# Kernel optimization log

Measured on AMD Instinct MI355X. Metric: run time of the kernel, lower is better.

## Reference

```python
import jax, jax.numpy as jnp
import numpy as np

D_MODEL = 1024
N_HEADS = 16
HEAD_DIM = D_MODEL // N_HEADS
B, T = 4, 2048
EPS = 1e-5


def _layernorm(x, w, b):
    mu = jnp.mean(x, axis=-1, keepdims=True)
    var = jnp.mean(jnp.square(x - mu), axis=-1, keepdims=True)
    return (x - mu) * jax.lax.rsqrt(var + EPS) * w + b


def _heads(x, w, b):
    # x: [B,T,D]; w stored [in,out] so y = x @ w + b (== torch Linear)
    y = x @ w + b
    return y.reshape(B, T, N_HEADS, HEAD_DIM).transpose(0, 2, 1, 3)  # [B,H,T,hd]


def _attention(q, k, v):
    scores = jnp.einsum('bhqd,bhkd->bhqk', q, k) / np.sqrt(HEAD_DIM).astype(np.float32)
    attn = jax.nn.softmax(scores, axis=-1)  # dropout is identity in eval mode
    o = jnp.einsum('bhqk,bhkd->bhqd', attn, v)
    return o.transpose(0, 2, 1, 3).reshape(B, T, D_MODEL)


def setup_inputs() -> dict:
    key = jax.random.key(0)
    ks = jax.random.split(key, 16)
    s = 1.0 / np.sqrt(D_MODEL)
    def lin(k, din, dout):
        kw, kb = jax.random.split(k)
        return (jax.random.uniform(kw, (din, dout), jnp.float32, -s, s),
                jax.random.uniform(kb, (dout,), jnp.float32, -s, s))
    inp = {}
    inp['temporal_tokens'] = jax.random.normal(ks[0], (B, T, D_MODEL), jnp.float32)
    inp['feature_tokens'] = jax.random.normal(ks[1], (B, T, D_MODEL), jnp.float32)
    names = ['qt', 'kf', 'vf', 'qf', 'kt', 'vt', 'ot', 'of']
    for i, n in enumerate(names):
        w, b = lin(ks[2 + i], D_MODEL, D_MODEL)
        inp[n + '_w'], inp[n + '_b'] = w, b
    inp['fus1_w'], inp['fus1_b'] = lin(ks[10], 2 * D_MODEL, D_MODEL)
    inp['fus2_w'], inp['fus2_b'] = lin(ks[11], D_MODEL, D_MODEL)
    for n in ['ln_fus', 'ln_t', 'ln_f']:
        inp[n + '_w'] = jnp.ones((D_MODEL,), jnp.float32)
        inp[n + '_b'] = jnp.zeros((D_MODEL,), jnp.float32)
    return inp


def reference(temporal_tokens, feature_tokens,
              qt_w, qt_b, kf_w, kf_b, vf_w, vf_b,
              qf_w, qf_b, kt_w, kt_b, vt_w, vt_b,
              ot_w, ot_b, of_w, of_b,
              fus1_w, fus1_b, fus2_w, fus2_b,
              ln_fus_w, ln_fus_b, ln_t_w, ln_t_b, ln_f_w, ln_f_b):
    # temporal -> feature cross attention
    Qt = _heads(temporal_tokens, qt_w, qt_b)
    Kf = _heads(feature_tokens, kf_w, kf_b)
    Vf = _heads(feature_tokens, vf_w, vf_b)
    attn_t = _attention(Qt, Kf, Vf) @ ot_w + ot_b
    fused_t = _layernorm(temporal_tokens + attn_t, ln_t_w, ln_t_b)
    # feature -> temporal cross attention
    Qf = _heads(feature_tokens, qf_w, qf_b)
    Kt = _heads(temporal_tokens, kt_w, kt_b)
    Vt = _heads(temporal_tokens, vt_w, vt_b)
    attn_f = _attention(Qf, Kt, Vt) @ of_w + of_b
    fused_f = _layernorm(feature_tokens + attn_f, ln_f_w, ln_f_b)
    # fusion MLP
    combined = jnp.concatenate([fused_t, fused_f], axis=-1)  # [B,T,2D]
    h = jax.nn.gelu(combined @ fus1_w + fus1_b, approximate=False)
    fused = _layernorm(h @ fus2_w + fus2_b, ln_fus_w, ln_fus_b)
    return fused
```

## Files before the change

### kernel.cpp

```cpp
#include <hip/hip_runtime.h>
#include <math.h>

typedef __attribute__((ext_vector_type(8))) short short8;
typedef __attribute__((ext_vector_type(4))) short short4v;
typedef __attribute__((ext_vector_type(4))) float floatx4;
typedef __attribute__((ext_vector_type(16))) float floatx16;

#define GLOBAL_AS __attribute__((address_space(1)))
#define LDS_AS __attribute__((address_space(3)))

__device__ __forceinline__ float bf2f(unsigned short u) {
    unsigned int x = ((unsigned int)u) << 16;
    return __builtin_bit_cast(float, x);
}
__device__ __forceinline__ unsigned short f2bf(float f) {
    unsigned int u = __builtin_bit_cast(unsigned int, f);
    u += 0x7fffu + ((u >> 16) & 1u);
    return (unsigned short)(u >> 16);
}

struct WX {
    const float* src[10];
    unsigned long long dst[10];
    int r64[10];
    int cum[11];
};

__global__ __launch_bounds__(256) void prep_kernel(
    WX P, unsigned short* __restrict__ base,
    const float* __restrict__ ta, const float* __restrict__ tb,
    unsigned short* __restrict__ oa, unsigned short* __restrict__ ob)
{
    __shared__ unsigned short T[64][72];
    const int bx = blockIdx.x;
    if (bx >= P.cum[10]) {
        const int cb = bx - P.cum[10];
        const float* in = cb < 1024 ? ta : tb;
        unsigned short* out = cb < 1024 ? oa : ob;
        const size_t b0 = (size_t)(cb & 1023) * 8192;
        #pragma unroll
        for (int j = 0; j < 8; ++j) {
            const size_t i = b0 + (size_t)j * 1024 + threadIdx.x * 4;
            float4 f = *(const float4*)(in + i);
            unsigned short o[4] = {f2bf(f.x), f2bf(f.y), f2bf(f.z), f2bf(f.w)};
            *(uint2*)(out + i) = *(const uint2*)o;
        }
        return;
    }
    int w = 0;
    #pragma unroll
    for (int i = 0; i < 10; ++i) if (bx >= P.cum[i + 1]) w = i + 1;
    const int tix = bx - P.cum[w];
    const int R = P.r64[w] * 64;
    const int r0 = (tix >> 4) * 64, c0 = (tix & 15) * 64;
    const float* in = P.src[w];
    unsigned short* out = base + P.dst[w];
    const int t = threadIdx.x;
    {
        const int r = t >> 2, cc = (t & 3) * 16;
        const float* p = in + (size_t)(r0 + r) * 1024 + c0 + cc;
        #pragma unroll
        for (int j = 0; j < 16; j += 4) {
            float4 f = *(const float4*)(p + j);
            T[cc + j + 0][r] = f2bf(f.x);
            T[cc + j + 1][r] = f2bf(f.y);
            T[cc + j + 2][r] = f2bf(f.z);
            T[cc + j + 3][r] = f2bf(f.w);
        }
    }
    __syncthreads();
    {
        const int c = t >> 2, rr = (t & 3) * 16;
        unsigned short* q = out + (size_t)(c0 + c) * R + r0 + rr;
        *(uint4*)(q)     = *(const uint4*)(&T[c][rr]);
        *(uint4*)(q + 8) = *(const uint4*)(&T[c][rr + 8]);
    }
}

#define G256_DECL(A_, B_, Kdim)                                               \
    const int tid = threadIdx.x;                                              \
    const int wave = tid >> 6, lane = tid & 63;                               \
    const int quad = lane >> 4, l16 = lane & 15;                              \
    const int wr = wave >> 2, wc = wave & 3;                                  \
    const int lrow8 = lane >> 3, lc8 = lane & 7;                              \
    floatx4 acc[8][4];                                                        \
    _Pragma("unroll")                                                         \
    for (int i = 0; i < 8; ++i)                                               \
        _Pragma("unroll")                                                     \
        for (int j = 0; j < 4; ++j) acc[i][j] = (floatx4){0.f, 0.f, 0.f, 0.f}; \
    const unsigned short* sA[4];                                              \
    const unsigned short* sB[4];                                              \
    int ldst[4];                                                              \
    _Pragma("unroll")                                                         \
    for (int h = 0; h < 2; ++h)                                               \
        _Pragma("unroll")                                                     \
        for (int j = 0; j < 2; ++j) {                                         \
            const int r0 = h * 128 + j * 64 + wave * 8;                       \
            const int r = r0 + lrow8;                                         \
            const int cg = lc8 ^ (r & 7);                                     \
            sA[h * 2 + j] = (A_) + (size_t)(bm + r) * (Kdim) + cg * 8;        \
            sB[h * 2 + j] = (B_) + (size_t)(bn + r) * (Kdim) + cg * 8;        \
            ldst[h * 2 + j] = r0 * 64;                                        \
        }

#define G256_STG_A(s_) __builtin_amdgcn_global_load_lds(                      \
    (const GLOBAL_AS void*)(sA[s_] + ko), (LDS_AS void*)(L + cb + ldst[s_]), 16, 0, 0)
#define G256_STG_B(s_) __builtin_amdgcn_global_load_lds(                      \
    (const GLOBAL_AS void*)(sB[s_] + ko), (LDS_AS void*)(L + cb + 16384 + ldst[s_]), 16, 0, 0)

#define G256_LDA(mh_)                                                         \
    _Pragma("unroll")                                                         \
    for (int mi = 0; mi < 4; ++mi) {                                          \
        const int r = (mh_) * 128 + wr * 64 + mi * 16 + l16;                  \
        _Pragma("unroll")                                                     \
        for (int kk = 0; kk < 2; ++kk)                                        \
            afc[mi][kk] = *(const short8*)&L[cb + r * 64 +                    \
                (((kk * 4 + quad) ^ (r & 7)) * 8)];                           \
    }
#define G256_LDB(nh_)                                                         \
    _Pragma("unroll")                                                         \
    for (int nj = 0; nj < 2; ++nj) {                                          \
        const int r = (nh_) * 128 + wc * 32 + nj * 16 + l16;                  \
        _Pragma("unroll")                                                     \
        for (int kk = 0; kk < 2; ++kk)                                        \
            bfr[(nh_) * 2 + nj][kk] = *(const short8*)&L[cb + 16384 + r * 64 +\
                (((kk * 4 + quad) ^ (r & 7)) * 8)];                           \
    }

#define G256_FENCE() do {                                                     \
    asm volatile("s_waitcnt lgkmcnt(0)" ::: "memory");                        \
    __builtin_amdgcn_sched_barrier(0);                                        \
    __builtin_amdgcn_s_barrier(); } while (0)

#define G256_MM(mh_, nb_) do {                                                \
    __builtin_amdgcn_s_setprio(1);                                            \
    _Pragma("unroll")                                                         \
    for (int mi = 0; mi < 4; ++mi)                                            \
        _Pragma("unroll")                                                     \
        for (int nj = 0; nj < 2; ++nj)                                        \
            _Pragma("unroll")                                                 \
            for (int kk = 0; kk < 2; ++kk)                                    \
                acc[(mh_) * 4 + mi][(nb_) + nj] =                             \
                    __builtin_amdgcn_mfma_f32_16x16x32_bf16(                  \
                        bfr[(nb_) + nj][kk], afc[mi][kk],                     \
                        acc[(mh_) * 4 + mi][(nb_) + nj], 0, 0, 0);            \
    __builtin_amdgcn_s_setprio(0); } while (0)

#define G256_CORE(A_, B_, Kdim)                                               \
    G256_DECL(A_, B_, Kdim)                                                   \
    {                       \
        _Pragma("unroll")                                                     \
        for (int s = 0; s < 4; ++s) {                                         \
            __builtin_amdgcn_global_load_lds((const GLOBAL_AS void*)(sA[s]),  \
                (LDS_AS void*)(L + ldst[s]), 16, 0, 0);                       \
            __builtin_amdgcn_global_load_lds((const GLOBAL_AS void*)(sB[s]),  \
                (LDS_AS void*)(L + 16384 + ldst[s]), 16, 0, 0);               \
        }                                                                     \
        _Pragma("unroll")                                                     \
        for (int s = 0; s < 4; ++s) {                                         \
            __builtin_amdgcn_global_load_lds((const GLOBAL_AS void*)(sA[s] + 64), \
                (LDS_AS void*)(L + 32768 + ldst[s]), 16, 0, 0);               \
            __builtin_amdgcn_global_load_lds((const GLOBAL_AS void*)(sB[s] + 64), \
                (LDS_AS void*)(L + 32768 + 16384 + ldst[s]), 16, 0, 0);       \
        }                                                                     \
        asm volatile("s_waitcnt vmcnt(8)" ::: "memory");                      \
        __builtin_amdgcn_s_barrier();                                         \
    }                                                                         \
    short8 afc[4][2];                                                         \
    short8 bfr[4][2];                                                         \
    const int NT = (Kdim) >> 6;                                               \
    for (int t = 0; t < NT; ++t) {                                            \
        const int cb = (t & 1) << 15;                                         \
        const int ko = (t + 2) << 6;                                          \
        const bool stg = (t < NT - 2);                                        \
                                                                      \
        G256_LDA(0)                                                           \
        G256_LDB(0)                                                           \
        G256_FENCE();                                                         \
        G256_MM(0, 0);                                                        \
                                                                      \
        G256_LDB(1)                                                           \
        if (stg) { G256_STG_A(0); G256_STG_A(1); G256_STG_B(0); G256_STG_B(1); } \
        G256_FENCE();                                                         \
        G256_MM(0, 2);                                                        \
                                                                      \
        G256_LDA(1)                                                           \
        if (stg) { G256_STG_B(2); G256_STG_B(3); }                            \
        G256_FENCE();                                                         \
        G256_MM(1, 2);                                                        \
                                                                      \
        if (stg) {                                                            \
            G256_STG_A(2); G256_STG_A(3);                                     \
            asm volatile("s_waitcnt vmcnt(8)" ::: "memory");                  \
        } else {                                                              \
            asm volatile("s_waitcnt vmcnt(0)" ::: "memory");                  \
        }                                                                     \
        __builtin_amdgcn_sched_barrier(0);                                    \
        __builtin_amdgcn_s_barrier();                                         \
        G256_MM(1, 0);                                                        \
    }


template <int MODE>
__global__ __launch_bounds__(512, 2) void gemm_kernel(
    const unsigned short* __restrict__ A,
    const unsigned short* __restrict__ Wt,
    const float* __restrict__ bias,
    unsigned short* __restrict__ C,
    int N, int K)
{
    __shared__ unsigned short L[65536];
    const int bm = blockIdx.x * 256, bn = blockIdx.y * 256;
    G256_CORE(A, Wt, K)

    #pragma unroll
    for (int i = 0; i < 8; ++i) {
        const int m = bm + (i >> 2) * 128 + wr * 64 + (i & 3) * 16 + l16;
        #pragma unroll
        for (int j = 0; j < 4; ++j) {
            const int n0 = bn + (j >> 1) * 128 + wc * 32 + (j & 1) * 16 + quad * 4;
            float4 bv = *(const float4*)&bias[n0];
            float v[4];
            #pragma unroll
            for (int r = 0; r < 4; ++r)
                v[r] = acc[i][j][r] + ((const float*)&bv)[r];
            if (MODE == 2) {
                #pragma unroll
                for (int r = 0; r < 4; ++r)
                    v[r] = 0.5f * v[r] * (1.0f + erff(v[r] * 0.70710678118f));
            }
            unsigned short o[4] = {f2bf(v[0]), f2bf(v[1]), f2bf(v[2]), f2bf(v[3])};
            *(uint2*)&C[(size_t)m * N + n0] = *(const uint2*)o;
        }
    }
}

__global__ __launch_bounds__(512, 2) void gemm_out_kernel(
    const unsigned short* __restrict__ A0, const unsigned short* __restrict__ W0,
    const float* __restrict__ bi0, const float* __restrict__ r0, unsigned short* __restrict__ C0,
    const unsigned short* __restrict__ A1, const unsigned short* __restrict__ W1,
    const float* __restrict__ bi1, const float* __restrict__ r1, unsigned short* __restrict__ C1)
{
    __shared__ unsigned short L[65536];
    const int s1 = blockIdx.y >> 2;
    const unsigned short* A = s1 ? A1 : A0;
    const unsigned short* Wt = s1 ? W1 : W0;
    const float* bias = s1 ? bi1 : bi0;
    const float* resid = s1 ? r1 : r0;
    unsigned short* C = s1 ? C1 : C0;
    const int bm = blockIdx.x * 256, bn = (blockIdx.y & 3) * 256;
    G256_CORE(A, Wt, 1024)

    #pragma unroll
    for (int i = 0; i < 8; ++i) {
        const int m = bm + (i >> 2) * 128 + wr * 64 + (i & 3) * 16 + l16;
        #pragma unroll
        for (int j = 0; j < 4; ++j) {
            const int n0 = bn + (j >> 1) * 128 + wc * 32 + (j & 1) * 16 + quad * 4;
            float4 bv = *(const float4*)&bias[n0];
            float4 rv = *(const float4*)&resid[(size_t)m * 1024 + n0];
            float v[4];
            v[0] = acc[i][j][0] + bv.x + rv.x;
            v[1] = acc[i][j][1] + bv.y + rv.y;
            v[2] = acc[i][j][2] + bv.z + rv.z;
            v[3] = acc[i][j][3] + bv.w + rv.w;
            unsigned short o[4] = {f2bf(v[0]), f2bf(v[1]), f2bf(v[2]), f2bf(v[3])};
            *(uint2*)&C[(size_t)m * 1024 + n0] = *(const uint2*)o;
        }
    }
}

__global__ __launch_bounds__(512, 2) void gemm_qkv_kernel(
    const unsigned short* __restrict__ At, const unsigned short* __restrict__ Wt3t,
    const float* __restrict__ tb0, const float* __restrict__ tb1, const float* __restrict__ tb2,
    unsigned short* __restrict__ to0, unsigned short* __restrict__ to1, unsigned short* __restrict__ to2,
    const unsigned short* __restrict__ Af, const unsigned short* __restrict__ Wt3f,
    const float* __restrict__ fb0, const float* __restrict__ fb1, const float* __restrict__ fb2,
    unsigned short* __restrict__ fo0, unsigned short* __restrict__ fo1, unsigned short* __restrict__ fo2,
    float scale0)
{
    __shared__ unsigned short L[65536];
    const int str = blockIdx.y >= 12;
    const unsigned short* A = str ? Af : At;
    const unsigned short* Wt = str ? Wt3f : Wt3t;
    const int byy = str ? (blockIdx.y - 12) : blockIdx.y;
    const int buf = byy >> 2;
    const int bn = byy * 256;
    const int cn = (byy & 3) * 256;
    const float* bias = str ? (buf == 0 ? fb0 : (buf == 1 ? fb1 : fb2))
                            : (buf == 0 ? tb0 : (buf == 1 ? tb1 : tb2));
    unsigned short* C = str ? (buf == 0 ? fo0 : (buf == 1 ? fo1 : fo2))
                            : (buf == 0 ? to0 : (buf == 1 ? to1 : to2));
    const float scale = buf == 0 ? scale0 : 1.0f;
    const int bm = blockIdx.x * 256;
    G256_CORE(A, Wt, 1024)

    #pragma unroll
    for (int i = 0; i < 8; ++i) {
        const int m = bm + (i >> 2) * 128 + wr * 64 + (i & 3) * 16 + l16;
        #pragma unroll
        for (int j = 0; j < 4; ++j) {
            const int n0 = cn + (j >> 1) * 128 + wc * 32 + (j & 1) * 16 + quad * 4;
            float4 bv = *(const float4*)&bias[n0];
            unsigned short o[4];
            #pragma unroll
            for (int r = 0; r < 4; ++r)
                o[r] = f2bf((acc[i][j][r] + ((const float*)&bv)[r]) * scale);
            if (buf == 2) {
                const int b = m >> 11, tk = m & 2047;
                const int h = n0 >> 6, d0 = n0 & 63;
                const int tsw = tk ^ ((d0 & 8) ? 4 : 0);
                unsigned short* vb = C + ((size_t)(b * 16 + h) * 64) * 2048 + tsw;
                #pragma unroll
                for (int r = 0; r < 4; ++r) vb[(size_t)(d0 + r) * 2048] = o[r];
            } else {
                *(uint2*)&C[(size_t)m * 1024 + n0] = *(const uint2*)o;
            }
        }
    }
}

__global__ __launch_bounds__(256) void flash_kernel(
    const unsigned short* __restrict__ Q0, const unsigned short* __restrict__ K0,
    const unsigned short* __restrict__ V0, unsigned short* __restrict__ O0,
    const unsigned short* __restrict__ Q1, const unsigned short* __restrict__ K1,
    const unsigned short* __restrict__ V1, unsigned short* __restrict__ O1)
{
    __shared__ unsigned short Ks[64 * 64];
    __shared__ unsigned short Vs[64 * 64];

    const int bid = blockIdx.x;
    const int p = (bid & 7) * 16 + (bid >> 7);
    const int qt = (bid >> 3) & 15;
    const int s1 = p >= 64;
    const int rem = p & 63;
    const int b = rem >> 4, h = rem & 15;
    const unsigned short* Q = s1 ? Q1 : Q0;
    const unsigned short* Kmat = s1 ? K1 : K0;
    const unsigned short* Vtp = s1 ? V1 : V0;
    unsigned short* O = s1 ? O1 : O0;
    const int q0 = qt * 128;

    const int tid = threadIdx.x;
    const int wave = tid >> 6, lane = tid & 63;
    const int quad = lane >> 4, l16 = lane & 15;

    const unsigned short* qp = Q + (size_t)(b * 2048 + q0 + wave * 32 + l16) * 1024 + h * 64;
    short8 qf[2][2];
    qf[0][0] = *(const short8*)(qp + quad * 8);
    qf[0][1] = *(const short8*)(qp + 32 + quad * 8);
    qf[1][0] = *(const short8*)(qp + 16 * 1024 + quad * 8);
    qf[1][1] = *(const short8*)(qp + 16 * 1024 + 32 + quad * 8);

    const int srow8 = lane >> 3;
    const int c8 = lane & 7;
    const int rit0 = wave * 16 + srow8;
    const int rit1 = rit0 + 8;
    const int col0 = (c8 ^ (rit0 & 7)) * 8;
    const int col1 = (c8 ^ (rit1 & 7)) * 8;
    const unsigned short* kbase = Kmat + (size_t)b * 2048 * 1024 + h * 64;
    const unsigned short* vbase = Vtp + (size_t)(b * 16 + h) * 64 * 2048;
    unsigned short* lk0 = Ks + (wave * 16) * 64;
    unsigned short* lk1 = lk0 + 8 * 64;
    unsigned short* lv0 = Vs + (wave * 16) * 64;
    unsigned short* lv1 = lv0 + 8 * 64;

    int koff[4][2];
    #pragma unroll
    for (int nt = 0; nt < 4; ++nt)
        #pragma unroll
        for (int hh = 0; hh < 2; ++hh)
            koff[nt][hh] = (nt * 16 + l16) * 64 + (((hh * 4 + quad) ^ (l16 & 7)) * 8);
    int voff[4][4];
    #pragma unroll
    for (int dt = 0; dt < 4; ++dt)
        #pragma unroll
        for (int nt = 0; nt < 4; ++nt)
            voff[dt][nt] = (dt * 16 + l16) * 64 +
                           (((nt * 2 + (quad >> 1)) ^ (l16 & 7)) * 8) +
                           (((quad & 1) ^ (l16 >> 3)) * 4);

    floatx4 oa[2][4], la[2];
    #pragma unroll
    for (int qg = 0; qg < 2; ++qg) {
        la[qg] = (floatx4){0.f, 0.f, 0.f, 0.f};
        #pragma unroll
        for (int dt = 0; dt < 4; ++dt) oa[qg][dt] = (floatx4){0.f, 0.f, 0.f, 0.f};
    }
    const short4v vone = {(short)0x3F80, (short)0x3F80, (short)0x3F80, (short)0x3F80};

    for (int kt = 0; kt < 32; ++kt) {
        const unsigned short* kg0 = kbase + (size_t)(kt * 64 + rit0) * 1024 + col0;
        const unsigned short* kg1 = kbase + (size_t)(kt * 64 + rit1) * 1024 + col1;
        const unsigned short* vg0 = vbase + (size_t)rit0 * 2048 + kt * 64 + col0;
        const unsigned short* vg1 = vbase + (size_t)rit1 * 2048 + kt * 64 + col1;
        __builtin_amdgcn_global_load_lds((const GLOBAL_AS void*)kg0, (LDS_AS void*)lk0, 16, 0, 0);
        __builtin_amdgcn_global_load_lds((const GLOBAL_AS void*)kg1, (LDS_AS void*)lk1, 16, 0, 0);
        __builtin_amdgcn_global_load_lds((const GLOBAL_AS void*)vg0, (LDS_AS void*)lv0, 16, 0, 0);
        __builtin_amdgcn_global_load_lds((const GLOBAL_AS void*)vg1, (LDS_AS void*)lv1, 16, 0, 0);
        __syncthreads();

        short4v pf[2][4];
        #pragma unroll
        for (int nt = 0; nt < 4; ++nt) {
            short8 k0 = *(const short8*)&Ks[koff[nt][0]];
            short8 k1 = *(const short8*)&Ks[koff[nt][1]];
            #pragma unroll
            for (int qg = 0; qg < 2; ++qg) {
                floatx4 s = (floatx4){0.f, 0.f, 0.f, 0.f};
                s = __builtin_amdgcn_mfma_f32_16x16x32_bf16(k0, qf[qg][0], s, 0, 0, 0);
                s = __builtin_amdgcn_mfma_f32_16x16x32_bf16(k1, qf[qg][1], s, 0, 0, 0);
                float p0 = __builtin_amdgcn_exp2f(s[0]);
                float p1 = __builtin_amdgcn_exp2f(s[1]);
                float p2 = __builtin_amdgcn_exp2f(s[2]);
                float p3 = __builtin_amdgcn_exp2f(s[3]);
                union { unsigned u[2]; short4v s4; } pk;
                asm("v_cvt_pk_bf16_f32 %0, %1, %2"
                    : "=v"(pk.u[0]) : "v"(p0), "v"(p1));
                asm("v_cvt_pk_bf16_f32 %0, %1, %2"
                    : "=v"(pk.u[1]) : "v"(p2), "v"(p3));
                pf[qg][nt] = pk.s4;
                la[qg] = __builtin_amdgcn_mfma_f32_16x16x16bf16_1k(vone, pf[qg][nt], la[qg], 0, 0, 0);
            }
        }
        #pragma unroll
        for (int dt = 0; dt < 4; ++dt)
            #pragma unroll
            for (int nt = 0; nt < 4; ++nt) {
                short4v vf = *(const short4v*)&Vs[voff[dt][nt]];
                oa[0][dt] = __builtin_amdgcn_mfma_f32_16x16x16bf16_1k(vf, pf[0][nt], oa[0][dt], 0, 0, 0);
                oa[1][dt] = __builtin_amdgcn_mfma_f32_16x16x16bf16_1k(vf, pf[1][nt], oa[1][dt], 0, 0, 0);
            }
        __syncthreads();
    }

    #pragma unroll
    for (int qg = 0; qg < 2; ++qg) {
        const float linv = 1.0f / la[qg][0];
        unsigned short* orow = O + (size_t)(b * 2048 + q0 + wave * 32 + qg * 16 + l16) * 1024 + h * 64;
        #pragma unroll
        for (int dt = 0; dt < 4; ++dt) {
            unsigned short ob[4];
            #pragma unroll
            for (int r = 0; r < 4; ++r) ob[r] = f2bf(oa[qg][dt][r] * linv);
            *(uint2*)(orow + dt * 16 + quad * 4) = *(const uint2*)ob;
        }
    }
}

__global__ __launch_bounds__(256) void ln2_kernel(
    const unsigned short* __restrict__ in0, const unsigned short* __restrict__ in1,
    unsigned short* __restrict__ out,
    const float* __restrict__ w0, const float* __restrict__ b0,
    const float* __restrict__ w1, const float* __restrict__ b1)
{
    __shared__ float red[8];
    const int sel = blockIdx.x >> 13;
    const int row = blockIdx.x & 8191;
    const unsigned short* in = sel ? in1 : in0;
    const float* w = sel ? w1 : w0;
    const float* bb = sel ? b1 : b0;
    const int tid = threadIdx.x;
    const int wave = tid >> 6, lane = tid & 63;
    uint2 raw = *(const uint2*)(in + (size_t)row * 1024 + tid * 4);
    float v[4];
    v[0] = bf2f((unsigned short)(raw.x & 0xffffu));
    v[1] = bf2f((unsigned short)(raw.x >> 16));
    v[2] = bf2f((unsigned short)(raw.y & 0xffffu));
    v[3] = bf2f((unsigned short)(raw.y >> 16));
    float s = v[0] + v[1] + v[2] + v[3];
    float sq = v[0] * v[0] + v[1] * v[1] + v[2] * v[2] + v[3] * v[3];
    #pragma unroll
    for (int m = 1; m < 64; m <<= 1) { s += __shfl_xor(s, m); sq += __shfl_xor(sq, m); }
    if (lane == 0) { red[wave] = s; red[4 + wave] = sq; }
    __syncthreads();
    s = red[0] + red[1] + red[2] + red[3];
    sq = red[4] + red[5] + red[6] + red[7];
    const float mu = s * (1.0f / 1024.0f);
    const float var = sq * (1.0f / 1024.0f) - mu * mu;
    const float rstd = rsqrtf(var + 1e-5f);
    unsigned short ob[4];
    #pragma unroll
    for (int j = 0; j < 4; ++j)
        ob[j] = f2bf((v[j] - mu) * rstd * w[tid * 4 + j] + bb[tid * 4 + j]);
    *(uint2*)(out + (size_t)row * 2048 + sel * 1024 + tid * 4) = *(uint2*)ob;
}

__global__ __launch_bounds__(256) void ln_final_kernel(
    const unsigned short* __restrict__ in, float* __restrict__ out,
    const float* __restrict__ w, const float* __restrict__ bias)
{
    __shared__ float red[8];
    const int row = blockIdx.x;
    const int tid = threadIdx.x;
    const int wave = tid >> 6, lane = tid & 63;
    uint2 raw = *(const uint2*)(in + (size_t)row * 1024 + tid * 4);
    float v[4];
    v[0] = bf2f((unsigned short)(raw.x & 0xffffu));
    v[1] = bf2f((unsigned short)(raw.x >> 16));
    v[2] = bf2f((unsigned short)(raw.y & 0xffffu));
    v[3] = bf2f((unsigned short)(raw.y >> 16));
    float s = v[0] + v[1] + v[2] + v[3];
    float sq = v[0] * v[0] + v[1] * v[1] + v[2] * v[2] + v[3] * v[3];
    #pragma unroll
    for (int m = 1; m < 64; m <<= 1) { s += __shfl_xor(s, m); sq += __shfl_xor(sq, m); }
    if (lane == 0) { red[wave] = s; red[4 + wave] = sq; }
    __syncthreads();
    s = red[0] + red[1] + red[2] + red[3];
    sq = red[4] + red[5] + red[6] + red[7];
    const float mu = s * (1.0f / 1024.0f);
    const float var = sq * (1.0f / 1024.0f) - mu * mu;
    const float rstd = rsqrtf(var + 1e-5f);
    float o[4];
    #pragma unroll
    for (int j = 0; j < 4; ++j)
        o[j] = (v[j] - mu) * rstd * w[tid * 4 + j] + bias[tid * 4 + j];
    *(float4*)(out + (size_t)row * 1024 + tid * 4) = (float4){o[0], o[1], o[2], o[3]};
}

extern "C" void kernel_launch(void* const* d_in, const int* in_sizes, int n_in,
                              void* d_out, int out_size, void* d_ws, size_t ws_size,
                              hipStream_t stream)
{
    (void)in_sizes; (void)n_in; (void)out_size; (void)ws_size;
    const float* temporal = (const float*)d_in[0];
    const float* feature  = (const float*)d_in[1];
    const float* qt_w = (const float*)d_in[2];
    const float* qt_b = (const float*)d_in[3];
    const float* kf_w = (const float*)d_in[4];
    const float* kf_b = (const float*)d_in[5];
    const float* vf_w = (const float*)d_in[6];
    const float* vf_b = (const float*)d_in[7];
    const float* qf_w = (const float*)d_in[8];
    const float* qf_b = (const float*)d_in[9];
    const float* kt_w = (const float*)d_in[10];
    const float* kt_b = (const float*)d_in[11];
    const float* vt_w = (const float*)d_in[12];
    const float* vt_b = (const float*)d_in[13];
    const float* ot_w = (const float*)d_in[14];
    const float* ot_b = (const float*)d_in[15];
    const float* of_w = (const float*)d_in[16];
    const float* of_b = (const float*)d_in[17];
    const float* fus1_w = (const float*)d_in[18];
    const float* fus1_b = (const float*)d_in[19];
    const float* fus2_w = (const float*)d_in[20];
    const float* fus2_b = (const float*)d_in[21];
    const float* ln_fus_w = (const float*)d_in[22];
    const float* ln_fus_b = (const float*)d_in[23];
    const float* ln_t_w = (const float*)d_in[24];
    const float* ln_t_b = (const float*)d_in[25];
    const float* ln_f_w = (const float*)d_in[26];
    const float* ln_f_b = (const float*)d_in[27];

    unsigned short* p = (unsigned short*)d_ws;
    const size_t EW = 1024ull * 1024;
    const size_t ET = 8192ull * 1024;
    unsigned short* WT3t = p;
    unsigned short* WT3f = p + 3 * EW;
    unsigned short* WTot = p + 6 * EW;
    unsigned short* WTof = p + 7 * EW;
    unsigned short* WTf1 = p + 8 * EW;
    unsigned short* WTf2 = p + 10 * EW;
    size_t off = 11 * EW;
    unsigned short* Tb = p + off; off += ET;
    unsigned short* Fb = p + off; off += ET;
    unsigned short* Qt = p + off; off += ET;
    unsigned short* Kt = p + off; off += ET;
    unsigned short* Vt = p + off; off += ET;
    unsigned short* Qf = p + off; off += ET;
    unsigned short* Kf = p + off; off += ET;
    unsigned short* Vf = p + off; off += ET;
    unsigned short* VfT = p + off; off += ET;
    unsigned short* VtT = p + off; off += ET;
    unsigned short* attnT = p + off; off += ET;
    unsigned short* attnF = p + off; off += ET;
    unsigned short* yT = Qt;
    unsigned short* yF = Qf;
    unsigned short* comb = Kt;
    unsigned short* hbuf = Kf;
    unsigned short* y2 = Vf;
    (void)Vt;

    const float SC = 0.125f * 1.4426950408889634f;

    {
        WX P;
        const float* srcs[10] = {qt_w, kt_w, vt_w, qf_w, kf_w, vf_w,
                                 ot_w, of_w, fus1_w, fus2_w};
        unsigned long long dsts[10] = {
            0, EW, 2 * EW,
            3 * EW, 4 * EW, 5 * EW,
            6 * EW, 7 * EW, 8 * EW, 10 * EW};
        int cum = 0;
        P.cum[0] = 0;
        for (int i = 0; i < 10; ++i) {
            P.src[i] = srcs[i];
            P.dst[i] = dsts[i];
            P.r64[i] = (i == 8) ? 32 : 16;
            cum += P.r64[i] * 16;
            P.cum[i + 1] = cum;
        }
        prep_kernel<<<cum + 2048, 256, 0, stream>>>(P, p, temporal, feature, Tb, Fb);
    }

    const dim3 gb5(512);
    gemm_qkv_kernel<<<dim3(32, 24), gb5, 0, stream>>>(
        Tb, WT3t, qt_b, kt_b, vt_b, Qt, Kt, VtT,
        Fb, WT3f, qf_b, kf_b, vf_b, Qf, Kf, VfT, SC);
    flash_kernel<<<2048, dim3(256), 0, stream>>>(
        Qt, Kf, VfT, attnT, Qf, Kt, VtT, attnF);
    gemm_out_kernel<<<dim3(32, 8), gb5, 0, stream>>>(
        attnT, WTot, ot_b, temporal, yT,
        attnF, WTof, of_b, feature,  yF);
    ln2_kernel<<<16384, dim3(256), 0, stream>>>(yT, yF, comb, ln_t_w, ln_t_b, ln_f_w, ln_f_b);
    gemm_kernel<2><<<dim3(32, 4), gb5, 0, stream>>>(comb, WTf1, fus1_b, hbuf, 1024, 2048);
    gemm_kernel<0><<<dim3(32, 4), gb5, 0, stream>>>(hbuf, WTf2, fus2_b, y2, 1024, 1024);
    ln_final_kernel<<<8192, dim3(256), 0, stream>>>(y2, (float*)d_out, ln_fus_w, ln_fus_b);
}
```

Before: 660.3 us.

## Replace fusion MLP GEMMs with 128x128 tile kernel using 32x32 MFMA

The two fusion-MLP GEMMs move off the 256x256-tile, 512-thread pipelined core onto a new 128x128-tile, 256-thread kernel. It uses 32x32x16 bf16 MFMA, swizzled LDS and direct global-to-LDS loads. The grid grows from 128 to 512 blocks to fill the CUs better on these mid-sized GEMMs, but the new loop is single-buffered with no prefetch overlap. The flash kernel also replaces its precomputed per-tile K/V LDS offset arrays with base offsets plus a constant stride, which reduces register pressure.

Result: faster. 640.8 us, median of 3 (-3.0%).

```diff
diff --git a/kernel.cpp b/kernel.cpp
--- a/kernel.cpp
+++ b/kernel.cpp
@@ -74,6 +74,101 @@
         unsigned short* q = out + (size_t)(c0 + c) * R + r0 + rr;
         *(uint4*)(q)     = *(const uint4*)(&T[c][rr]);
         *(uint4*)(q + 8) = *(const uint4*)(&T[c][rr + 8]);
+    }
+}
+
+#define GEMM_CORE(A_, B_, Kdim)                                               \
+    const int tid = threadIdx.x;                                              \
+    const int wave = tid >> 6, lane = tid & 63;                               \
+    const int l32 = lane & 31, hi = lane >> 5;                                \
+    const int wm = (wave & 1) * 64, wn = (wave >> 1) * 64;                    \
+    const int srow8 = lane >> 3, c8 = lane & 7;                               \
+    const int scol = (c8 ^ srow8) * 8;                                        \
+    floatx16 acc[2][2];                                                       \
+    _Pragma("unroll")                                                         \
+    for (int i = 0; i < 2; ++i)                                               \
+        _Pragma("unroll")                                                     \
+        for (int j = 0; j < 2; ++j)                                           \
+            _Pragma("unroll")                                                 \
+            for (int r = 0; r < 16; ++r) acc[i][j][r] = 0.f;                  \
+    const unsigned short* pa[4];                                              \
+    const unsigned short* pb[4];                                              \
+    _Pragma("unroll")                                                         \
+    for (int i = 0; i < 4; ++i) {                                             \
+        pa[i] = (A_) + (size_t)(bm + i * 32 + wave * 8 + srow8) * (Kdim) + scol; \
+        pb[i] = (B_) + (size_t)(bn + i * 32 + wave * 8 + srow8) * (Kdim) + scol; \
+    }                                                                         \
+    int aoff[2][4], boff[2][4];                                               \
+    _Pragma("unroll")                                                         \
+    for (int f = 0; f < 2; ++f)                                               \
+        _Pragma("unroll")                                                     \
+        for (int s = 0; s < 4; ++s) {                                         \
+            const int cg = ((s * 2 + hi) ^ (l32 & 7)) * 8;                    \
+            aoff[f][s] = (wm + f * 32 + l32) * 64 + cg;                       \
+            boff[f][s] = (wn + f * 32 + l32) * 64 + cg;                       \
+        }                                                                     \
+    for (int k0 = 0; k0 < (Kdim); k0 += 64) {                                 \
+        _Pragma("unroll")                                                     \
+        for (int i = 0; i < 4; ++i) {                                         \
+            __builtin_amdgcn_global_load_lds((const GLOBAL_AS void*)(pa[i] + k0), \
+                (LDS_AS void*)(As + i * 2048 + wave * 512), 16, 0, 0);        \
+            __builtin_amdgcn_global_load_lds((const GLOBAL_AS void*)(pb[i] + k0), \
+                (LDS_AS void*)(Bs + i * 2048 + wave * 512), 16, 0, 0);        \
+        }                                                                     \
+        __syncthreads();                                                      \
+        _Pragma("unroll")                                                     \
+        for (int s = 0; s < 4; ++s) {                                         \
+            short8 af[2], bf[2];                                              \
+            _Pragma("unroll")                                                 \
+            for (int f = 0; f < 2; ++f) {                                     \
+                af[f] = *(const short8*)&As[aoff[f][s]];                      \
+                bf[f] = *(const short8*)&Bs[boff[f][s]];                      \
+            }                                                                 \
+            _Pragma("unroll")                                                 \
+            for (int mi = 0; mi < 2; ++mi)                                    \
+                _Pragma("unroll")                                             \
+                for (int ni = 0; ni < 2; ++ni)                                \
+                    acc[mi][ni] = __builtin_amdgcn_mfma_f32_32x32x16_bf16(    \
+                        bf[ni], af[mi], acc[mi][ni], 0, 0, 0);                \
+        }                                                                     \
+        __syncthreads();                                                      \
+    }
+
+template <int MODE>
+__global__ __launch_bounds__(256) void gemm_kernel(
+    const unsigned short* __restrict__ A,
+    const unsigned short* __restrict__ Wt,
+    const float* __restrict__ bias,
+    unsigned short* __restrict__ C,
+    int N, int K)
+{
+    __shared__ unsigned short As[128 * 64];
+    __shared__ unsigned short Bs[128 * 64];
+    const int bm = blockIdx.x * 128, bn = blockIdx.y * 128;
+    GEMM_CORE(A, Wt, K)
+
+    #pragma unroll
+    for (int mi = 0; mi < 2; ++mi) {
+        const int m = bm + wm + mi * 32 + l32;
+        #pragma unroll
+        for (int ni = 0; ni < 2; ++ni) {
+            #pragma unroll
+            for (int rg = 0; rg < 4; ++rg) {
+                const int n0 = bn + wn + ni * 32 + rg * 8 + hi * 4;
+                float4 bv = *(const float4*)&bias[n0];
+                float v[4];
+                #pragma unroll
+                for (int r = 0; r < 4; ++r)
+                    v[r] = acc[mi][ni][rg * 4 + r] + ((const float*)&bv)[r];
+                if (MODE == 2) {
+                    #pragma unroll
+                    for (int r = 0; r < 4; ++r)
+                        v[r] = 0.5f * v[r] * (1.0f + erff(v[r] * 0.70710678118f));
+                }
+                unsigned short o[4] = {f2bf(v[0]), f2bf(v[1]), f2bf(v[2]), f2bf(v[3])};
+                *(uint2*)&C[(size_t)m * N + n0] = *(const uint2*)o;
+            }
+        }
     }
 }
 
@@ -200,41 +295,6 @@
         G256_MM(1, 0);                                                        \
     }
 
-
-template <int MODE>
-__global__ __launch_bounds__(512, 2) void gemm_kernel(
-    const unsigned short* __restrict__ A,
-    const unsigned short* __restrict__ Wt,
-    const float* __restrict__ bias,
-    unsigned short* __restrict__ C,
-    int N, int K)
-{
-    __shared__ unsigned short L[65536];
-    const int bm = blockIdx.x * 256, bn = blockIdx.y * 256;
-    G256_CORE(A, Wt, K)
-
-    #pragma unroll
-    for (int i = 0; i < 8; ++i) {
-        const int m = bm + (i >> 2) * 128 + wr * 64 + (i & 3) * 16 + l16;
-        #pragma unroll
-        for (int j = 0; j < 4; ++j) {
-            const int n0 = bn + (j >> 1) * 128 + wc * 32 + (j & 1) * 16 + quad * 4;
-            float4 bv = *(const float4*)&bias[n0];
-            float v[4];
-            #pragma unroll
-            for (int r = 0; r < 4; ++r)
-                v[r] = acc[i][j][r] + ((const float*)&bv)[r];
-            if (MODE == 2) {
-                #pragma unroll
-                for (int r = 0; r < 4; ++r)
-                    v[r] = 0.5f * v[r] * (1.0f + erff(v[r] * 0.70710678118f));
-            }
-            unsigned short o[4] = {f2bf(v[0]), f2bf(v[1]), f2bf(v[2]), f2bf(v[3])};
-            *(uint2*)&C[(size_t)m * N + n0] = *(const uint2*)o;
-        }
-    }
-}
-
 __global__ __launch_bounds__(512, 2) void gemm_out_kernel(
     const unsigned short* __restrict__ A0, const unsigned short* __restrict__ W0,
     const float* __restrict__ bi0, const float* __restrict__ r0, unsigned short* __restrict__ C0,
@@ -365,20 +425,13 @@
     unsigned short* lv0 = Vs + (wave * 16) * 64;
     unsigned short* lv1 = lv0 + 8 * 64;
 
-    int koff[4][2];
+    const int kb0 = l16 * 64 + ((quad ^ (l16 & 7)) * 8);
+    const int kb1 = l16 * 64 + (((4 + quad) ^ (l16 & 7)) * 8);
+    const int vbq = ((quad & 1) ^ (l16 >> 3)) * 4;
+    int vb[4];
     #pragma unroll
     for (int nt = 0; nt < 4; ++nt)
-        #pragma unroll
-        for (int hh = 0; hh < 2; ++hh)
-            koff[nt][hh] = (nt * 16 + l16) * 64 + (((hh * 4 + quad) ^ (l16 & 7)) * 8);
-    int voff[4][4];
-    #pragma unroll
-    for (int dt = 0; dt < 4; ++dt)
-        #pragma unroll
-        for (int nt = 0; nt < 4; ++nt)
-            voff[dt][nt] = (dt * 16 + l16) * 64 +
-                           (((nt * 2 + (quad >> 1)) ^ (l16 & 7)) * 8) +
-                           (((quad & 1) ^ (l16 >> 3)) * 4);
+        vb[nt] = l16 * 64 + (((nt * 2 + (quad >> 1)) ^ (l16 & 7)) * 8) + vbq;
 
     floatx4 oa[2][4], la[2];
     #pragma unroll
@@ -403,8 +456,8 @@
         short4v pf[2][4];
         #pragma unroll
         for (int nt = 0; nt < 4; ++nt) {
-            short8 k0 = *(const short8*)&Ks[koff[nt][0]];
-            short8 k1 = *(const short8*)&Ks[koff[nt][1]];
+            short8 k0 = *(const short8*)&Ks[nt * 1024 + kb0];
+            short8 k1 = *(const short8*)&Ks[nt * 1024 + kb1];
             #pragma unroll
             for (int qg = 0; qg < 2; ++qg) {
                 floatx4 s = (floatx4){0.f, 0.f, 0.f, 0.f};
@@ -427,7 +480,7 @@
         for (int dt = 0; dt < 4; ++dt)
             #pragma unroll
             for (int nt = 0; nt < 4; ++nt) {
-                short4v vf = *(const short4v*)&Vs[voff[dt][nt]];
+                short4v vf = *(const short4v*)&Vs[dt * 1024 + vb[nt]];
                 oa[0][dt] = __builtin_amdgcn_mfma_f32_16x16x16bf16_1k(vf, pf[0][nt], oa[0][dt], 0, 0, 0);
                 oa[1][dt] = __builtin_amdgcn_mfma_f32_16x16x16bf16_1k(vf, pf[1][nt], oa[1][dt], 0, 0, 0);
             }
@@ -613,7 +666,7 @@
         attnT, WTot, ot_b, temporal, yT,
         attnF, WTof, of_b, feature,  yF);
     ln2_kernel<<<16384, dim3(256), 0, stream>>>(yT, yF, comb, ln_t_w, ln_t_b, ln_f_w, ln_f_b);
-    gemm_kernel<2><<<dim3(32, 4), gb5, 0, stream>>>(comb, WTf1, fus1_b, hbuf, 1024, 2048);
-    gemm_kernel<0><<<dim3(32, 4), gb5, 0, stream>>>(hbuf, WTf2, fus2_b, y2, 1024, 1024);
+    gemm_kernel<2><<<dim3(64, 8), dim3(256), 0, stream>>>(comb, WTf1, fus1_b, hbuf, 1024, 2048);
+    gemm_kernel<0><<<dim3(64, 8), dim3(256), 0, stream>>>(hbuf, WTf2, fus2_b, y2, 1024, 1024);
     ln_final_kernel<<<8192, dim3(256), 0, stream>>>(y2, (float*)d_out, ln_fus_w, ln_fus_b);
 }
```
